# Optimization experiments

Measured on AMD Instinct MI355X. Metric: run time of the kernel, lower is better.

## Reference

```python
import jax, jax.numpy as jnp
import numpy as np

# Model hyperparameters (from init_kwargs)
D_MODEL, D_STATE, D_CONV, EXPAND, NHEADS, NGROUPS = 1024, 16, 4, 2, 8, 1
D_INNER = D_MODEL * EXPAND                      # 2048
HEADDIM = D_INNER // NHEADS                     # 256
D_XBC = D_INNER + 2 * NGROUPS * D_STATE         # conv channels: x + B + C
D_IN_PROJ = 3 * D_INNER + D_XBC + NHEADS        # z0 + x0 + z(unused) + xBC + dt
BATCH, SEQLEN = 2, 2048
LN_EPS = 1e-5


def setup_inputs() -> dict:
    key = jax.random.key(0)
    ks = jax.random.split(key, 8)
    u = jax.random.normal(ks[0], (BATCH, SEQLEN, D_MODEL), dtype=jnp.float32)
    W_in = jax.random.normal(ks[1], (D_IN_PROJ, D_MODEL), jnp.float32) / np.sqrt(D_MODEL)
    conv_w = jax.random.normal(ks[2], (D_XBC, 1, D_CONV), jnp.float32) / np.sqrt(D_CONV)
    conv_b = jnp.zeros((D_XBC,), jnp.float32)
    # dt_bias = inverse-softplus of dt ~ LogUniform(1e-3, 1e-1), as in source init
    dt = jnp.exp(jax.random.uniform(ks[3], (NHEADS,)) * (np.log(0.1) - np.log(0.001)) + np.log(0.001))
    dt_bias = dt + jnp.log(-jnp.expm1(-dt))
    A_log = jnp.log(jax.random.uniform(ks[4], (NHEADS,), minval=0.9, maxval=0.999))
    D_param = jnp.ones((NHEADS,), jnp.float32)
    ln_gamma = jnp.ones((D_INNER,), jnp.float32)
    ln_beta = jnp.zeros((D_INNER,), jnp.float32)
    W_gate = jax.random.normal(ks[5], (D_INNER, D_INNER), jnp.float32) / np.sqrt(D_INNER)
    b_gate = jnp.zeros((D_INNER,), jnp.float32)
    W_out = jax.random.normal(ks[6], (D_MODEL, 2 * D_INNER), jnp.float32) / np.sqrt(2 * D_INNER)
    return dict(u=u, W_in=W_in, conv_w=conv_w, conv_b=conv_b, dt_bias=dt_bias,
                A_log=A_log, D_param=D_param, ln_gamma=ln_gamma, ln_beta=ln_beta,
                W_gate=W_gate, b_gate=b_gate, W_out=W_out)


def _silu(x):
    return x * jax.nn.sigmoid(x)


def reference(u, W_in, conv_w, conv_b, dt_bias, A_log, D_param,
              ln_gamma, ln_beta, W_gate, b_gate, W_out):
    B, L, _ = u.shape
    zxbcdt = u @ W_in.T                                   # [B,L,D_IN_PROJ]
    z0 = zxbcdt[..., :D_INNER]
    x0 = zxbcdt[..., D_INNER:2 * D_INNER]
    # z = zxbcdt[..., 2*D_INNER:3*D_INNER]  # split but never used in source forward
    xBC = zxbcdt[..., 3 * D_INNER:3 * D_INNER + D_XBC]
    dt = jax.nn.softplus(zxbcdt[..., -NHEADS:] + dt_bias)  # [B,L,H]
    A = -jnp.exp(A_log)                                    # [H], per-head scalar

    # causal depthwise conv1d over time (left pad d_conv-1, crop to L)
    xBC_c = jnp.transpose(xBC, (0, 2, 1))                  # [B,C,L]
    xBC_c = jax.lax.conv_general_dilated(
        xBC_c, conv_w, window_strides=(1,), padding=[(D_CONV - 1, 0)],
        dimension_numbers=('NCH', 'OIH', 'NCH'), feature_group_count=D_XBC)
    xBC = _silu(jnp.transpose(xBC_c, (0, 2, 1)) + conv_b)  # [B,L,C]

    x = xBC[..., :D_INNER].reshape(B, L, NHEADS, HEADDIM)  # [B,L,H,P]
    Bm = xBC[..., D_INNER:D_INNER + D_STATE]               # [B,L,N] (ngroups=1)
    Cm = xBC[..., D_INNER + D_STATE:]                      # [B,L,N]

    def step(h, inp):
        x_t, B_t, C_t, dt_t = inp                          # [B,H,P],[B,N],[B,N],[B,H]
        dA = jnp.exp(dt_t * A)[:, :, None, None]           # [B,H,1,1]
        h = dA * h + (dt_t[:, :, None, None] * x_t[..., None]) * B_t[:, None, None, :]
        y_t = jnp.einsum('bhpn,bn->bhp', h, C_t) + D_param[None, :, None] * x_t
        return h, y_t

    h0 = jnp.zeros((B, NHEADS, HEADDIM, D_STATE), u.dtype)
    xs = (jnp.moveaxis(x, 1, 0), jnp.moveaxis(Bm, 1, 0),
          jnp.moveaxis(Cm, 1, 0), jnp.moveaxis(dt, 1, 0))
    _, y = jax.lax.scan(step, h0, xs)                      # [L,B,H,P]
    y = jnp.moveaxis(y, 0, 1).reshape(B, L, D_INNER)

    # LayerNorm
    mu = y.mean(-1, keepdims=True)
    var = ((y - mu) ** 2).mean(-1, keepdims=True)
    y = (y - mu) * jax.lax.rsqrt(var + LN_EPS) * ln_gamma + ln_beta

    gate = jax.nn.sigmoid(y @ W_gate.T + b_gate)
    y = gate * y

    mlp_skip = _silu(z0) * x0
    return jnp.concatenate([mlp_skip, y], axis=-1) @ W_out.T  # [B,L,D_MODEL]
```

## Files before the change

### kernel.cpp

```cpp
#include <hip/hip_runtime.h>
#include <hip/hip_bf16.h>
#include <math.h>

#define BATCH   2
#define SEQLEN  2048
#define DMODEL  1024
#define DINNER  2048
#define DSTATE  16
#define NHEADS  8
#define HEADDIM 256
#define DXBC    2080
#define NPACK   6184
#define NPAD    6400
#define MROWS   4096
#define CHUNK   64
#define NCHUNK  32
#define BH      16

typedef unsigned int u32;
typedef unsigned short u16;
typedef __attribute__((ext_vector_type(8))) short short8;
typedef __attribute__((ext_vector_type(4))) float f32x4;

#define GLOAD16(g, l) __builtin_amdgcn_global_load_lds( \
    (const __attribute__((address_space(1))) u32*)(g),  \
    (__attribute__((address_space(3))) u32*)(l), 16, 0, 0)

__device__ __forceinline__ u16 f2bf(float f) {
  union { float f; u32 u; } v; v.f = f;
  u32 r = v.u + 0x7fff + ((v.u >> 16) & 1);
  return (u16)(r >> 16);
}
__device__ __forceinline__ float bf2f(u16 b) {
  union { u32 u; float f; } v; v.u = ((u32)b) << 16;
  return v.f;
}

struct GParts { float* p0; float* p1; };

#define S_U   1048576
#define S_WG  1048576
#define S_WO  1048576
#define S_WP  1638400
#define S_TOT (S_U + S_WG + S_WO + S_WP)

__global__ void cvt_all(const float* __restrict__ u, const float* __restrict__ Wg,
                        const float* __restrict__ Wo, const float* __restrict__ Win,
                        u16* __restrict__ ub, u16* __restrict__ Wgb,
                        u16* __restrict__ Wob, u16* __restrict__ Wp) {
  for (int i = blockIdx.x * 256 + threadIdx.x; i < S_TOT; i += gridDim.x * 256) {
    const float* src; u16* dst; int idx;
    if (i < S_U) { src = u; dst = ub; idx = i; }
    else if (i < S_U + S_WG) { src = Wg; dst = Wgb; idx = i - S_U; }
    else if (i < S_U + S_WG + S_WO) { src = Wo; dst = Wob; idx = i - S_U - S_WG; }
    else {
      int j = i - S_U - S_WG - S_WO;
      int row = j >> 8, c4 = j & 255;
      ushort4 o = make_ushort4(0, 0, 0, 0);
      if (row < NPACK) {
        int orig = row < 4096 ? row : row + 2048;
        float4 v = ((const float4*)(Win + (size_t)orig * DMODEL))[c4];
        o = make_ushort4(f2bf(v.x), f2bf(v.y), f2bf(v.z), f2bf(v.w));
      }
      ((ushort4*)Wp)[j] = o;
      continue;
    }
    float4 v = ((const float4*)src)[idx];
    ((ushort4*)dst)[idx] = make_ushort4(f2bf(v.x), f2bf(v.y), f2bf(v.z), f2bf(v.w));
  }
}


template <int BMT>
__device__ __forceinline__ void stage32(const u16* __restrict__ Ag,
                                        const u16* __restrict__ Bg,
                                        int ldk, char* buf, int w, int l) {
  const int rr = w * 16 + (l >> 2);
  const int kc = (l & 3) * 8;
  #pragma unroll
  for (int j = 0; j < BMT / 128; ++j)
    GLOAD16(Ag + (size_t)(j * 128 + rr) * ldk + kc, buf + j * 8192 + w * 1024);
  #pragma unroll
  for (int j = 0; j < 2; ++j)
    GLOAD16(Bg + (size_t)(j * 128 + rr) * ldk + kc, buf + BMT * 64 + j * 8192 + w * 1024);
}

template <int EPI, int BMT>
__global__ __launch_bounds__(512, 1) void gemm256(
    const u16* __restrict__ A, const u16* __restrict__ B, int K_loop, int ldk, int ldo,
    void* __restrict__ outp, const float* __restrict__ bias,
    const u16* __restrict__ gate_in, GParts gp) {
  constexpr int ABYTES = BMT * 64;
  constexpr int TBYTES = ABYTES + 16384;
  constexpr int MREP   = BMT / 32;
  __shared__ char lds[4 * TBYTES];
  const int tid = threadIdx.x;
  const int w = tid >> 6, l = tid & 63;
  const int wm = w >> 2, wn = w & 3;
  const int fr = l & 15, g = l >> 4;
  int s = blockIdx.y * gridDim.x + blockIdx.x;
  const int nwg = gridDim.x * gridDim.y;
  s = (s & 7) * (nwg >> 3) + (s >> 3);
  const int bx = s % gridDim.x, by = s / gridDim.x;
  const u16* Ap = A + (size_t)bx * BMT * ldk + (size_t)blockIdx.z * K_loop;
  const u16* Bp = B + (size_t)by * 256 * ldk + (size_t)blockIdx.z * K_loop;
  const int NT = K_loop >> 5;

  f32x4 acc[MREP][4];
  #pragma unroll
  for (int m = 0; m < MREP; ++m)
    #pragma unroll
    for (int n = 0; n < 4; ++n) acc[m][n] = (f32x4){0.f, 0.f, 0.f, 0.f};

  stage32<BMT>(Ap,      Bp,      ldk, lds,              w, l);
  stage32<BMT>(Ap + 32, Bp + 32, ldk, lds + TBYTES,     w, l);
  stage32<BMT>(Ap + 64, Bp + 64, ldk, lds + 2 * TBYTES, w, l);
  if constexpr (BMT == 256) asm volatile("s_waitcnt vmcnt(8)" ::: "memory");
  else                      asm volatile("s_waitcnt vmcnt(6)" ::: "memory");
  __builtin_amdgcn_s_barrier();
  __builtin_amdgcn_sched_barrier(0);

  auto compute = [&](int t) {
    const char* cb = lds + (t & 3) * TBYTES;
    short8 bf[4];
    #pragma unroll
    for (int n = 0; n < 4; ++n)
      bf[n] = *(const short8*)(cb + ABYTES + (wn * 64 + n * 16 + fr) * 64 + g * 16);
    #pragma unroll
    for (int m = 0; m < MREP; ++m) {
      short8 am = *(const short8*)(cb + (wm * (BMT / 2) + m * 16 + fr) * 64 + g * 16);
      #pragma unroll
      for (int n = 0; n < 4; ++n)
        acc[m][n] = __builtin_amdgcn_mfma_f32_16x16x32_bf16(am, bf[n], acc[m][n], 0, 0, 0);
    }
  };

  int t = 0;
  for (; t < NT - 3; ++t) {
    stage32<BMT>(Ap + (size_t)(t + 3) * 32, Bp + (size_t)(t + 3) * 32, ldk,
                 lds + ((t + 3) & 3) * TBYTES, w, l);
    __builtin_amdgcn_sched_barrier(0);
    compute(t);
    if constexpr (BMT == 256) asm volatile("s_waitcnt vmcnt(8)" ::: "memory");
    else                      asm volatile("s_waitcnt vmcnt(6)" ::: "memory");
    __builtin_amdgcn_s_barrier();
    __builtin_amdgcn_sched_barrier(0);
  }
  compute(t);
  if constexpr (BMT == 256) asm volatile("s_waitcnt vmcnt(4)" ::: "memory");
  else                      asm volatile("s_waitcnt vmcnt(3)" ::: "memory");
  __builtin_amdgcn_s_barrier();
  __builtin_amdgcn_sched_barrier(0);
  compute(t + 1);
  asm volatile("s_waitcnt vmcnt(0)" ::: "memory");
  __builtin_amdgcn_s_barrier();
  __builtin_amdgcn_sched_barrier(0);
  compute(t + 2);

  const int er = (l >> 4) * 4, ec = l & 15;
  float* pp = nullptr;
  if (EPI == 2) pp = blockIdx.z == 0 ? gp.p0 : gp.p1;
  #pragma unroll
  for (int m = 0; m < MREP; ++m) {
    #pragma unroll
    for (int n = 0; n < 4; ++n) {
      #pragma unroll
      for (int j = 0; j < 4; ++j) {
        int row = bx * BMT + wm * (BMT / 2) + m * 16 + er + j;
        int col = by * 256 + wn * 64 + n * 16 + ec;
        float v = acc[m][n][j];
        if (EPI == 0) {
          ((u16*)outp)[(size_t)row * ldo + col] = f2bf(v);
        } else if (EPI == 1) {
          float gt = 1.f / (1.f + __expf(-(v + bias[col])));
          float nv = bf2f(gate_in[(size_t)row * 2048 + col]);
          ((u16*)outp)[(size_t)row * 4096 + 2048 + col] = f2bf(gt * nv);
        } else {
          pp[(size_t)row * ldo + col] = v;
        }
      }
    }
  }
}

__global__ void reduce2(const float* __restrict__ p0, const float* __restrict__ p1,
                        float* __restrict__ out) {
  const int n4 = MROWS * DMODEL / 4;
  for (int i = blockIdx.x * 256 + threadIdx.x; i < n4; i += gridDim.x * 256) {
    float4 a = ((const float4*)p0)[i];
    float4 b = ((const float4*)p1)[i];
    float4 o;
    o.x = a.x + b.x; o.y = a.y + b.y; o.z = a.z + b.z; o.w = a.w + b.w;
    ((float4*)out)[i] = o;
  }
}

#define NB_CONV 33280
#define NB_MLP  8192
#define NB_DT   128

__global__ void prep_kernel(const u16* __restrict__ zx, const float* __restrict__ cw,
                            const float* __restrict__ cb, u16* __restrict__ xc,
                            float* __restrict__ bc, u16* __restrict__ hcat,
                            const float* __restrict__ dt_bias, float* __restrict__ dtb) {
  int blk = blockIdx.x;
  if (blk < NB_CONV) {
    int idx = blk * 256 + threadIdx.x;
    if (idx >= MROWS * DXBC) return;
    int c = idx % DXBC;
    int m = idx / DXBC;
    int l = m & (SEQLEN - 1);
    float acc = cb[c];
    float w0 = cw[c * 4 + 0], w1 = cw[c * 4 + 1], w2 = cw[c * 4 + 2], w3 = cw[c * 4 + 3];
    const u16* col = zx + (size_t)m * NPAD + 4096 + c;
    acc += w3 * bf2f(col[0]);
    if (l >= 1) acc += w2 * bf2f(col[-NPAD]);
    if (l >= 2) acc += w1 * bf2f(col[-2 * NPAD]);
    if (l >= 3) acc += w0 * bf2f(col[-3 * NPAD]);
    float sv = acc / (1.f + __expf(-acc));
    if (c < DINNER) xc[(size_t)m * DINNER + c] = f2bf(sv);
    else bc[(size_t)m * 32 + (c - DINNER)] = sv;
  } else if (blk < NB_CONV + NB_MLP) {
    int i = (blk - NB_CONV) * 256 + threadIdx.x;
    int m = i >> 9, c4 = (i & 511) * 4;
    const u16* row = zx + (size_t)m * NPAD;
    ushort4 zv = *(const ushort4*)(row + c4);
    ushort4 xv = *(const ushort4*)(row + 2048 + c4);
    float z0, x0;
    ushort4 o;
    z0 = bf2f(zv.x); x0 = bf2f(xv.x); o.x = f2bf(x0 * z0 / (1.f + __expf(-z0)));
    z0 = bf2f(zv.y); x0 = bf2f(xv.y); o.y = f2bf(x0 * z0 / (1.f + __expf(-z0)));
    z0 = bf2f(zv.z); x0 = bf2f(xv.z); o.z = f2bf(x0 * z0 / (1.f + __expf(-z0)));
    z0 = bf2f(zv.w); x0 = bf2f(xv.w); o.w = f2bf(x0 * z0 / (1.f + __expf(-z0)));
    *(ushort4*)(hcat + (size_t)m * 4096 + c4) = o;
  } else {
    int idx = (blk - NB_CONV - NB_MLP) * 256 + threadIdx.x;
    if (idx >= MROWS * NHEADS) return;
    int hd = idx & 7, m = idx >> 3;
    float raw = bf2f(zx[(size_t)m * NPAD + 6176 + hd]) + dt_bias[hd];
    float dtv = raw > 20.f ? raw : log1pf(expf(raw));
    dtb[idx] = dtv;
  }
}

__device__ __forceinline__ int xs_addr(int r, int p) {
  return r * 512 + ((((p >> 3) ^ ((r >> 3) & 3)) & 31) << 4) + (p & 7) * 2;
}
__device__ __forceinline__ int P_addr(int t, int s) {
  return t * 128 + ((((s >> 3) ^ (t & 7)) & 7) << 4) + (s & 7) * 2;
}

__device__ __forceinline__ void stage_x(u16* xs, const u16* __restrict__ xc,
                                        size_t base, int tid) {
  #pragma unroll
  for (int it = 0; it < 8; ++it) {
    int r = it * 8 + (tid >> 5);
    int pc = (tid & 31) * 8;
    short8 v = *(const short8*)(xc + base + (size_t)r * DINNER + pc);
    *(short8*)((char*)xs + xs_addr(r, pc)) = v;
  }
}

__device__ __forceinline__ short8 xfrag(const u16* xs, int k0, int g, int p) {
  short8 v;
  #pragma unroll
  for (int j = 0; j < 8; ++j) {
    int s = k0 + g * 8 + j;
    v[j] = *(const short*)((const char*)xs + xs_addr(s, p));
  }
  return v;
}

__global__ __launch_bounds__(256) void ssd_state(
    const u16* __restrict__ xc, const float* __restrict__ bcb,
    const float* __restrict__ dtb, const float* __restrict__ A_log,
    float* __restrict__ Sbuf, float* __restrict__ lcbuf) {
  __shared__ u16 xs[64 * 256];
  __shared__ float sLC[64], sDT[64];
  __shared__ float wBT[16][65];
  const int tid = threadIdx.x;
  const int bh = blockIdx.x >> 5, c = blockIdx.x & 31;
  const int b = bh >> 3, h = bh & 7;
  const size_t row0 = (size_t)b * SEQLEN + c * CHUNK;
  stage_x(xs, xc, row0 * DINNER + h * HEADDIM, tid);
  if (tid < 64) {
    float dtv = dtb[(row0 + tid) * NHEADS + h];
    float A = -__expf(A_log[h]);
    float s = dtv * A;
    #pragma unroll
    for (int off = 1; off < 64; off <<= 1) {
      float v = __shfl_up(s, off, 64);
      if (tid >= off) s += v;
    }
    sLC[tid] = s; sDT[tid] = dtv;
    lcbuf[(size_t)blockIdx.x * 64 + tid] = s;
  }
  __syncthreads();
  const float lc63 = sLC[63];
  for (int i = tid; i < 1024; i += 256) {
    int n = i & 15, t = i >> 4;
    float w = sDT[t] * __expf(lc63 - sLC[t]);
    wBT[n][t] = w * bcb[(row0 + t) * 32 + n];
  }
  __syncthreads();
  const int lane = tid & 63, w = tid >> 6;
  const int cl = lane & 15, g = lane >> 4;
  f32x4 acc[4];
  #pragma unroll
  for (int pt = 0; pt < 4; ++pt) acc[pt] = (f32x4){0.f, 0.f, 0.f, 0.f};
  #pragma unroll
  for (int kk = 0; kk < 2; ++kk) {
    int k0 = kk * 32;
    short8 af;
    #pragma unroll
    for (int j = 0; j < 8; ++j) af[j] = (short)f2bf(wBT[cl][k0 + g * 8 + j]);
    #pragma unroll
    for (int pt = 0; pt < 4; ++pt) {
      short8 bf = xfrag(xs, k0, g, (w * 4 + pt) * 16 + cl);
      acc[pt] = __builtin_amdgcn_mfma_f32_16x16x32_bf16(af, bf, acc[pt], 0, 0, 0);
    }
  }
  float* Sc = Sbuf + (size_t)blockIdx.x * 16 * 256;
  #pragma unroll
  for (int pt = 0; pt < 4; ++pt)
    #pragma unroll
    for (int j = 0; j < 4; ++j)
      Sc[(g * 4 + j) * 256 + (w * 4 + pt) * 16 + cl] = acc[pt][j];
}

__global__ __launch_bounds__(256) void ssd_combine(
    const float* __restrict__ Sbuf, const float* __restrict__ lcbuf,
    float* __restrict__ Sprev) {
  const int bh = blockIdx.x >> 4, seg = blockIdx.x & 15;
  const int idx = seg * 256 + threadIdx.x;
  float r = 0.f;
  #pragma unroll 1
  for (int c = 0; c < NCHUNK; ++c) {
    size_t o = ((size_t)bh * NCHUNK + c) * 4096 + idx;
    Sprev[o] = r;
    float lam = __expf(lcbuf[((size_t)bh * NCHUNK + c) * 64 + 63]);
    r = lam * r + Sbuf[o];
  }
}

__global__ __launch_bounds__(256) void ssd_out(
    const u16* __restrict__ xc, const float* __restrict__ bcb,
    const float* __restrict__ dtb, const float* __restrict__ lcbuf,
    const float* __restrict__ Sprev, const float* __restrict__ D_par,
    u16* __restrict__ y) {
  __shared__ u16 xs[64 * 256];
  __shared__ u16 P[64 * 64];
  __shared__ u16 sB[64][17], sC[64][17], sCe[64][17];
  __shared__ u16 sSp[256][17];
  __shared__ float sLC[64], sDT[64];
  const int tid = threadIdx.x;
  const int bh = blockIdx.x >> 5, c = blockIdx.x & 31;
  const int b = bh >> 3, h = bh & 7;
  const size_t row0 = (size_t)b * SEQLEN + c * CHUNK;
  stage_x(xs, xc, row0 * DINNER + h * HEADDIM, tid);
  if (tid < 64) {
    sLC[tid] = lcbuf[(size_t)blockIdx.x * 64 + tid];
    sDT[tid] = dtb[(row0 + tid) * NHEADS + h];
  }
  for (int i = tid; i < 1024; i += 256) {
    int n = i & 15, t = i >> 4;
    float Bv = bcb[(row0 + t) * 32 + n];
    float Cv = bcb[(row0 + t) * 32 + 16 + n];
    float e = __expf(lcbuf[(size_t)blockIdx.x * 64 + t]);
    sB[t][n] = f2bf(Bv);
    sC[t][n] = f2bf(Cv);
    sCe[t][n] = f2bf(Cv * e);
  }
  {
    const float* Sp = Sprev + (size_t)blockIdx.x * 4096;
    int p = tid & 255;
    if (tid < 256) {
      #pragma unroll
      for (int n = 0; n < 16; ++n) sSp[p][n] = f2bf(Sp[n * 256 + p]);
    }
  }
  __syncthreads();

  const int lane = tid & 63, w = tid >> 6;
  const int cl = lane & 15, g = lane >> 4;

  f32x4 gacc[4];
  #pragma unroll
  for (int st = 0; st < 4; ++st) gacc[st] = (f32x4){0.f, 0.f, 0.f, 0.f};
  short8 afc = (short8){0, 0, 0, 0, 0, 0, 0, 0};
  if (g < 2) {
    #pragma unroll
    for (int j = 0; j < 8; ++j) afc[j] = (short)sC[w * 16 + cl][g * 8 + j];
  }
  #pragma unroll
  for (int st = 0; st < 4; ++st) {
    short8 bfb = (short8){0, 0, 0, 0, 0, 0, 0, 0};
    if (g < 2) {
      #pragma unroll
      for (int j = 0; j < 8; ++j) bfb[j] = (short)sB[st * 16 + cl][g * 8 + j];
    }
    gacc[st] = __builtin_amdgcn_mfma_f32_16x16x32_bf16(afc, bfb, gacc[st], 0, 0, 0);
  }
  #pragma unroll
  for (int st = 0; st < 4; ++st) {
    #pragma unroll
    for (int j = 0; j < 4; ++j) {
      int t = w * 16 + g * 4 + j;
      int s = st * 16 + cl;
      float v = 0.f;
      if (s <= t) v = gacc[st][j] * sDT[s] * __expf(sLC[t] - sLC[s]);
      *(u16*)((char*)P + P_addr(t, s)) = f2bf(v);
    }
  }
  asm volatile("s_waitcnt lgkmcnt(0)" ::: "memory");
  __builtin_amdgcn_sched_barrier(0);

  f32x4 acc[16];
  #pragma unroll
  for (int pt = 0; pt < 16; ++pt) acc[pt] = (f32x4){0.f, 0.f, 0.f, 0.f};
  #pragma unroll
  for (int kk = 0; kk < 2; ++kk) {
    int k0 = kk * 32;
    short8 ap = *(const short8*)((const char*)P + P_addr(w * 16 + cl, k0 + g * 8));
    #pragma unroll
    for (int pt = 0; pt < 16; ++pt) {
      short8 bf = xfrag(xs, k0, g, pt * 16 + cl);
      acc[pt] = __builtin_amdgcn_mfma_f32_16x16x32_bf16(ap, bf, acc[pt], 0, 0, 0);
    }
  }
  {
    short8 ae = (short8){0, 0, 0, 0, 0, 0, 0, 0};
    if (g < 2) {
      #pragma unroll
      for (int j = 0; j < 8; ++j) ae[j] = (short)sCe[w * 16 + cl][g * 8 + j];
    }
    #pragma unroll
    for (int pt = 0; pt < 16; ++pt) {
      short8 bs = (short8){0, 0, 0, 0, 0, 0, 0, 0};
      if (g < 2) {
        #pragma unroll
        for (int j = 0; j < 8; ++j) bs[j] = (short)sSp[pt * 16 + cl][g * 8 + j];
      }
      acc[pt] = __builtin_amdgcn_mfma_f32_16x16x32_bf16(ae, bs, acc[pt], 0, 0, 0);
    }
  }
  const float Dv = D_par[h];
  #pragma unroll
  for (int pt = 0; pt < 16; ++pt) {
    #pragma unroll
    for (int j = 0; j < 4; ++j) {
      int t = w * 16 + g * 4 + j;
      int p = pt * 16 + cl;
      float xv = bf2f(*(const u16*)((const char*)xs + xs_addr(t, p)));
      float v = acc[pt][j] + Dv * xv;
      y[(row0 + t) * DINNER + h * HEADDIM + p] = f2bf(v);
    }
  }
}

__global__ __launch_bounds__(256) void ln_kernel(const u16* __restrict__ y,
                                                 const float* __restrict__ gamma,
                                                 const float* __restrict__ beta,
                                                 u16* __restrict__ nrm) {
  const int row = blockIdx.x;
  const int t = threadIdx.x;
  const u16* yr = y + (size_t)row * DINNER;
  short8 v = *(const short8*)(yr + t * 8);
  float f[8];
  float s = 0.f, ss = 0.f;
  #pragma unroll
  for (int j = 0; j < 8; ++j) {
    f[j] = bf2f((u16)v[j]);
    s += f[j]; ss += f[j] * f[j];
  }
  #pragma unroll
  for (int o = 1; o < 64; o <<= 1) { s += __shfl_xor(s, o); ss += __shfl_xor(ss, o); }
  __shared__ float rs[4], rss[4];
  const int wid = t >> 6;
  if ((t & 63) == 0) { rs[wid] = s; rss[wid] = ss; }
  __syncthreads();
  s = rs[0] + rs[1] + rs[2] + rs[3];
  ss = rss[0] + rss[1] + rss[2] + rss[3];
  float mu = s * (1.f / DINNER);
  float var = ss * (1.f / DINNER) - mu * mu;
  float inv = rsqrtf(var + 1e-5f);
  float4 g0 = ((const float4*)gamma)[t * 2], g1 = ((const float4*)gamma)[t * 2 + 1];
  float4 b0 = ((const float4*)beta)[t * 2], b1 = ((const float4*)beta)[t * 2 + 1];
  short8 o;
  o[0] = (short)f2bf((f[0] - mu) * inv * g0.x + b0.x);
  o[1] = (short)f2bf((f[1] - mu) * inv * g0.y + b0.y);
  o[2] = (short)f2bf((f[2] - mu) * inv * g0.z + b0.z);
  o[3] = (short)f2bf((f[3] - mu) * inv * g0.w + b0.w);
  o[4] = (short)f2bf((f[4] - mu) * inv * g1.x + b1.x);
  o[5] = (short)f2bf((f[5] - mu) * inv * g1.y + b1.y);
  o[6] = (short)f2bf((f[6] - mu) * inv * g1.z + b1.z);
  o[7] = (short)f2bf((f[7] - mu) * inv * g1.w + b1.w);
  *(short8*)(nrm + (size_t)row * DINNER + t * 8) = o;
}

extern "C" void kernel_launch(void* const* d_in, const int* in_sizes, int n_in,
                              void* d_out, int out_size, void* d_ws, size_t ws_size,
                              hipStream_t stream) {
  (void)in_sizes; (void)n_in; (void)out_size; (void)ws_size;
  const float* u       = (const float*)d_in[0];
  const float* W_in    = (const float*)d_in[1];
  const float* conv_w  = (const float*)d_in[2];
  const float* conv_b  = (const float*)d_in[3];
  const float* dt_bias = (const float*)d_in[4];
  const float* A_log   = (const float*)d_in[5];
  const float* D_par   = (const float*)d_in[6];
  const float* ln_g    = (const float*)d_in[7];
  const float* ln_b    = (const float*)d_in[8];
  const float* W_gate  = (const float*)d_in[9];
  const float* b_gate  = (const float*)d_in[10];
  const float* W_out   = (const float*)d_in[11];
  float* out = (float*)d_out;

  size_t off = 0;
  auto take = [&](size_t bytes) -> char* {
    char* p = (char*)d_ws + off;
    off = (off + bytes + 255) & ~(size_t)255;
    return p;
  };
  u16* u16b  = (u16*)take((size_t)MROWS * DMODEL * 2);
  u16* Wp    = (u16*)take((size_t)NPAD * DMODEL * 2);
  u16* Wg    = (u16*)take((size_t)DINNER * DINNER * 2);
  u16* Wo    = (u16*)take((size_t)DMODEL * 2 * DINNER * 2);
  u16* zx    = (u16*)take((size_t)MROWS * NPAD * 2);
  u16* xc    = (u16*)take((size_t)MROWS * DINNER * 2);
  float* bcb = (float*)take((size_t)MROWS * 32 * 4);
  float* dtb = (float*)take((size_t)MROWS * NHEADS * 4);
  float* lcbuf = (float*)take((size_t)BH * NCHUNK * 64 * 4);
  u16* nrm   = (u16*)take((size_t)MROWS * DINNER * 2);
  u16* hcat  = (u16*)take((size_t)MROWS * 2 * DINNER * 2);

  float* Sbuf  = (float*)u16b;
  u16*   y     = zx;
  float* Sprev = (float*)((char*)zx + (size_t)16 * 1024 * 1024);
  GParts parts2;
  parts2.p0 = (float*)zx;
  parts2.p1 = (float*)((char*)zx + (size_t)16 * 1024 * 1024);
  GParts none = {nullptr, nullptr};

  cvt_all<<<4096, 256, 0, stream>>>(u, W_gate, W_out, W_in, u16b, Wg, Wo, Wp);

  gemm256<0, 256><<<dim3(MROWS / 256, NPAD / 256, 1), 512, 0, stream>>>(
      u16b, Wp, DMODEL, DMODEL, NPAD, zx, nullptr, nullptr, none);

  prep_kernel<<<NB_CONV + NB_MLP + NB_DT, 256, 0, stream>>>(
      zx, conv_w, conv_b, xc, bcb, hcat, dt_bias, dtb);

  ssd_state<<<BH * NCHUNK, 256, 0, stream>>>(xc, bcb, dtb, A_log, Sbuf, lcbuf);
  ssd_combine<<<BH * 16, 256, 0, stream>>>(Sbuf, lcbuf, Sprev);
  ssd_out<<<BH * NCHUNK, 256, 0, stream>>>(xc, bcb, dtb, lcbuf, Sprev, D_par, y);

  ln_kernel<<<MROWS, 256, 0, stream>>>(y, ln_g, ln_b, nrm);

  gemm256<1, 128><<<dim3(MROWS / 128, DINNER / 256, 1), 512, 0, stream>>>(
      nrm, Wg, DINNER, DINNER, 0, hcat, b_gate, nrm, none);

  gemm256<2, 128><<<dim3(MROWS / 128, DMODEL / 256, 2), 512, 0, stream>>>(
      hcat, Wo, 2 * DINNER / 2, 2 * DINNER, DMODEL, nullptr, nullptr, nullptr, parts2);

  reduce2<<<2048, 256, 0, stream>>>(parts2.p0, parts2.p1, out);
}
```

Baseline: 256.9 us.

## Rewrite GEMM kernels with K=64 swizzled LDS tiles and interleaved staging

Replaces the generic 4-stage K=32 GEMM with two specialised kernels. The in-projection GEMM uses a double-buffered K=64 tile and an XOR-swizzled LDS layout. It interleaves global-to-LDS loads for the next tile between MFMA groups and raises wave priority during MFMA bursts. The gate and out-proj GEMMs switch to 256x128 tiles with a 3-stage K=64 pipeline. The aim is fewer barriers, fewer LDS bank conflicts and better load/compute overlap, at the cost of more complex vmcnt bookkeeping and a different wave tiling.

```diff
diff --git a/kernel.cpp b/kernel.cpp
--- a/kernel.cpp
+++ b/kernel.cpp
@@ -25,6 +25,8 @@
 #define GLOAD16(g, l) __builtin_amdgcn_global_load_lds( \
     (const __attribute__((address_space(1))) u32*)(g),  \
     (__attribute__((address_space(3))) u32*)(l), 16, 0, 0)
+
+#define MFMA_B16(d, a, b) d = __builtin_amdgcn_mfma_f32_16x16x32_bf16(a, b, d, 0, 0, 0)
 
 __device__ __forceinline__ u16 f2bf(float f) {
   union { float f; u32 u; } v; v.f = f;
@@ -70,30 +72,26 @@
   }
 }
 
-
-template <int BMT>
-__device__ __forceinline__ void stage32(const u16* __restrict__ Ag,
-                                        const u16* __restrict__ Bg,
-                                        int ldk, char* buf, int w, int l) {
-  const int rr = w * 16 + (l >> 2);
-  const int kc = (l & 3) * 8;
-  #pragma unroll
-  for (int j = 0; j < BMT / 128; ++j)
-    GLOAD16(Ag + (size_t)(j * 128 + rr) * ldk + kc, buf + j * 8192 + w * 1024);
-  #pragma unroll
-  for (int j = 0; j < 2; ++j)
-    GLOAD16(Bg + (size_t)(j * 128 + rr) * ldk + kc, buf + BMT * 64 + j * 8192 + w * 1024);
-}
-
-template <int EPI, int BMT>
-__global__ __launch_bounds__(512, 1) void gemm256(
-    const u16* __restrict__ A, const u16* __restrict__ B, int K_loop, int ldk, int ldo,
-    void* __restrict__ outp, const float* __restrict__ bias,
-    const u16* __restrict__ gate_in, GParts gp) {
-  constexpr int ABYTES = BMT * 64;
-  constexpr int TBYTES = ABYTES + 16384;
-  constexpr int MREP   = BMT / 32;
-  __shared__ char lds[4 * TBYTES];
+template <int NL>
+__device__ __forceinline__ void stage_rows(const u16* __restrict__ gsrc, int ldk,
+                                           char* ldsmat, int row0, int w, int l) {
+  const int rl = w * 8 + (l >> 3);
+  const int q = ((l & 7) ^ (l >> 3)) * 8;
+  #pragma unroll
+  for (int j = 0; j < NL; ++j) {
+    GLOAD16(gsrc + (size_t)(row0 + j * 64 + rl) * ldk + q,
+            ldsmat + (row0 + j * 64 + w * 8) * 128);
+  }
+}
+
+__device__ __forceinline__ short8 frag8(const char* mat, int row, int q) {
+  return *(const short8*)(mat + row * 128 + ((q ^ (row & 7)) << 4));
+}
+
+__global__ __launch_bounds__(512, 1) void gemmA(
+    const u16* __restrict__ A, const u16* __restrict__ B, int K, int ldk,
+    int ldo, u16* __restrict__ outp) {
+  __shared__ char lds[131072];
   const int tid = threadIdx.x;
   const int w = tid >> 6, l = tid & 63;
   const int wm = w >> 2, wn = w & 3;
@@ -102,76 +100,236 @@
   const int nwg = gridDim.x * gridDim.y;
   s = (s & 7) * (nwg >> 3) + (s >> 3);
   const int bx = s % gridDim.x, by = s / gridDim.x;
-  const u16* Ap = A + (size_t)bx * BMT * ldk + (size_t)blockIdx.z * K_loop;
-  const u16* Bp = B + (size_t)by * 256 * ldk + (size_t)blockIdx.z * K_loop;
-  const int NT = K_loop >> 5;
-
-  f32x4 acc[MREP][4];
-  #pragma unroll
-  for (int m = 0; m < MREP; ++m)
+  const u16* Ap = A + (size_t)bx * 256 * ldk;
+  const u16* Bp = B + (size_t)by * 256 * ldk;
+  const int NT = K >> 6;
+
+  f32x4 acc[8][4];
+  #pragma unroll
+  for (int m = 0; m < 8; ++m)
     #pragma unroll
     for (int n = 0; n < 4; ++n) acc[m][n] = (f32x4){0.f, 0.f, 0.f, 0.f};
 
-  stage32<BMT>(Ap,      Bp,      ldk, lds,              w, l);
-  stage32<BMT>(Ap + 32, Bp + 32, ldk, lds + TBYTES,     w, l);
-  stage32<BMT>(Ap + 64, Bp + 64, ldk, lds + 2 * TBYTES, w, l);
-  if constexpr (BMT == 256) asm volatile("s_waitcnt vmcnt(8)" ::: "memory");
-  else                      asm volatile("s_waitcnt vmcnt(6)" ::: "memory");
-  __builtin_amdgcn_s_barrier();
-  __builtin_amdgcn_sched_barrier(0);
-
-  auto compute = [&](int t) {
-    const char* cb = lds + (t & 3) * TBYTES;
-    short8 bf[4];
-    #pragma unroll
-    for (int n = 0; n < 4; ++n)
-      bf[n] = *(const short8*)(cb + ABYTES + (wn * 64 + n * 16 + fr) * 64 + g * 16);
-    #pragma unroll
-    for (int m = 0; m < MREP; ++m) {
-      short8 am = *(const short8*)(cb + (wm * (BMT / 2) + m * 16 + fr) * 64 + g * 16);
-      #pragma unroll
-      for (int n = 0; n < 4; ++n)
-        acc[m][n] = __builtin_amdgcn_mfma_f32_16x16x32_bf16(am, bf[n], acc[m][n], 0, 0, 0);
-    }
-  };
-
-  int t = 0;
-  for (; t < NT - 3; ++t) {
-    stage32<BMT>(Ap + (size_t)(t + 3) * 32, Bp + (size_t)(t + 3) * 32, ldk,
-                 lds + ((t + 3) & 3) * TBYTES, w, l);
-    __builtin_amdgcn_sched_barrier(0);
-    compute(t);
-    if constexpr (BMT == 256) asm volatile("s_waitcnt vmcnt(8)" ::: "memory");
-    else                      asm volatile("s_waitcnt vmcnt(6)" ::: "memory");
+  stage_rows<2>(Bp, ldk, lds + 32768, 0, w, l);
+  stage_rows<2>(Bp, ldk, lds + 32768, 128, w, l);
+  stage_rows<1>(Ap, ldk, lds, 0, w, l);
+  stage_rows<1>(Ap, ldk, lds, 128, w, l);
+  stage_rows<1>(Ap, ldk, lds, 64, w, l);
+  stage_rows<1>(Ap, ldk, lds, 192, w, l);
+
+  for (int t = 0; t < NT; ++t) {
+    const bool last = (t == NT - 1);
+    const char* cbA = lds + (t & 1) * 65536;
+    const char* cbB = cbA + 32768;
+    char* nbA = lds + ((t + 1) & 1) * 65536;
+    char* nbB = nbA + 32768;
+    const u16* An = Ap + (size_t)(t + 1) * 64;
+    const u16* Bn = Bp + (size_t)(t + 1) * 64;
+
+    asm volatile("s_waitcnt vmcnt(2)" ::: "memory");
     __builtin_amdgcn_s_barrier();
     __builtin_amdgcn_sched_barrier(0);
-  }
-  compute(t);
-  if constexpr (BMT == 256) asm volatile("s_waitcnt vmcnt(4)" ::: "memory");
-  else                      asm volatile("s_waitcnt vmcnt(3)" ::: "memory");
-  __builtin_amdgcn_s_barrier();
-  __builtin_amdgcn_sched_barrier(0);
-  compute(t + 1);
-  asm volatile("s_waitcnt vmcnt(0)" ::: "memory");
-  __builtin_amdgcn_s_barrier();
-  __builtin_amdgcn_sched_barrier(0);
-  compute(t + 2);
-
-  const int er = (l >> 4) * 4, ec = l & 15;
+
+    short8 bf0[4], bf1[4];
+    #pragma unroll
+    for (int n = 0; n < 4; ++n) {
+      bf0[n] = frag8(cbB, wn * 64 + n * 16 + fr, g);
+      bf1[n] = frag8(cbB, wn * 64 + n * 16 + fr, 4 + g);
+    }
+    {
+      short8 a00 = frag8(cbA, wm * 128 + fr, g);
+      short8 a01 = frag8(cbA, wm * 128 + fr, 4 + g);
+      short8 a10 = frag8(cbA, wm * 128 + 16 + fr, g);
+      short8 a11 = frag8(cbA, wm * 128 + 16 + fr, 4 + g);
+      if (!last) stage_rows<2>(Bn, ldk, nbB, 0, w, l);
+      asm volatile("s_waitcnt lgkmcnt(0)" ::: "memory");
+      __builtin_amdgcn_sched_barrier(0);
+      __builtin_amdgcn_s_setprio(1);
+      #pragma unroll
+      for (int n = 0; n < 4; ++n) { MFMA_B16(acc[0][n], a00, bf0[n]); MFMA_B16(acc[1][n], a10, bf0[n]); }
+      #pragma unroll
+      for (int n = 0; n < 4; ++n) { MFMA_B16(acc[0][n], a01, bf1[n]); MFMA_B16(acc[1][n], a11, bf1[n]); }
+      __builtin_amdgcn_s_setprio(0);
+    }
+    {
+      short8 a00 = frag8(cbA, wm * 128 + 32 + fr, g);
+      short8 a01 = frag8(cbA, wm * 128 + 32 + fr, 4 + g);
+      short8 a10 = frag8(cbA, wm * 128 + 48 + fr, g);
+      short8 a11 = frag8(cbA, wm * 128 + 48 + fr, 4 + g);
+      if (!last) stage_rows<2>(Bn, ldk, nbB, 128, w, l);
+      asm volatile("s_waitcnt lgkmcnt(0)" ::: "memory");
+      __builtin_amdgcn_sched_barrier(0);
+      __builtin_amdgcn_s_setprio(1);
+      #pragma unroll
+      for (int n = 0; n < 4; ++n) { MFMA_B16(acc[2][n], a00, bf0[n]); MFMA_B16(acc[3][n], a10, bf0[n]); }
+      #pragma unroll
+      for (int n = 0; n < 4; ++n) { MFMA_B16(acc[2][n], a01, bf1[n]); MFMA_B16(acc[3][n], a11, bf1[n]); }
+      __builtin_amdgcn_s_setprio(0);
+    }
+    if (last) { asm volatile("s_waitcnt vmcnt(0)" ::: "memory"); }
+    else      { asm volatile("s_waitcnt vmcnt(4)" ::: "memory"); }
+    __builtin_amdgcn_s_barrier();
+    __builtin_amdgcn_sched_barrier(0);
+    {
+      short8 a00 = frag8(cbA, wm * 128 + 64 + fr, g);
+      short8 a01 = frag8(cbA, wm * 128 + 64 + fr, 4 + g);
+      short8 a10 = frag8(cbA, wm * 128 + 80 + fr, g);
+      short8 a11 = frag8(cbA, wm * 128 + 80 + fr, 4 + g);
+      if (!last) { stage_rows<1>(An, ldk, nbA, 0, w, l); stage_rows<1>(An, ldk, nbA, 128, w, l); }
+      asm volatile("s_waitcnt lgkmcnt(0)" ::: "memory");
+      __builtin_amdgcn_sched_barrier(0);
+      __builtin_amdgcn_s_setprio(1);
+      #pragma unroll
+      for (int n = 0; n < 4; ++n) { MFMA_B16(acc[4][n], a00, bf0[n]); MFMA_B16(acc[5][n], a10, bf0[n]); }
+      #pragma unroll
+      for (int n = 0; n < 4; ++n) { MFMA_B16(acc[4][n], a01, bf1[n]); MFMA_B16(acc[5][n], a11, bf1[n]); }
+      __builtin_amdgcn_s_setprio(0);
+    }
+    {
+      short8 a00 = frag8(cbA, wm * 128 + 96 + fr, g);
+      short8 a01 = frag8(cbA, wm * 128 + 96 + fr, 4 + g);
+      short8 a10 = frag8(cbA, wm * 128 + 112 + fr, g);
+      short8 a11 = frag8(cbA, wm * 128 + 112 + fr, 4 + g);
+      if (!last) { stage_rows<1>(An, ldk, nbA, 64, w, l); stage_rows<1>(An, ldk, nbA, 192, w, l); }
+      asm volatile("s_waitcnt lgkmcnt(0)" ::: "memory");
+      __builtin_amdgcn_sched_barrier(0);
+      __builtin_amdgcn_s_setprio(1);
+      #pragma unroll
+      for (int n = 0; n < 4; ++n) { MFMA_B16(acc[6][n], a00, bf0[n]); MFMA_B16(acc[7][n], a10, bf0[n]); }
+      #pragma unroll
+      for (int n = 0; n < 4; ++n) { MFMA_B16(acc[6][n], a01, bf1[n]); MFMA_B16(acc[7][n], a11, bf1[n]); }
+      __builtin_amdgcn_s_setprio(0);
+    }
+  }
+
+  const int er = g * 4;
+  #pragma unroll
+  for (int m = 0; m < 8; ++m)
+    #pragma unroll
+    for (int n = 0; n < 4; ++n)
+      #pragma unroll
+      for (int j = 0; j < 4; ++j) {
+        int row = bx * 256 + wm * 128 + m * 16 + er + j;
+        int col = by * 256 + wn * 64 + n * 16 + fr;
+        outp[(size_t)row * ldo + col] = f2bf(acc[m][n][j]);
+      }
+}
+
+template <int EPI>
+__global__ __launch_bounds__(512, 1) void gemmB(
+    const u16* __restrict__ A, const u16* __restrict__ B, int K_loop, int ldk,
+    int ldo, void* __restrict__ outp, const float* __restrict__ bias,
+    const u16* __restrict__ gate_in, GParts gp) {
+  __shared__ char lds[3 * 49152];
+  const int tid = threadIdx.x;
+  const int w = tid >> 6, l = tid & 63;
+  const int wm = w >> 1, wn = w & 1;
+  const int fr = l & 15, g = l >> 4;
+  int s = blockIdx.y * gridDim.x + blockIdx.x;
+  const int nwg = gridDim.x * gridDim.y;
+  s = (s & 7) * (nwg >> 3) + (s >> 3);
+  const int bx = s % gridDim.x, by = s / gridDim.x;
+  const u16* Ap = A + (size_t)bx * 256 * ldk + (size_t)blockIdx.z * K_loop;
+  const u16* Bp = B + (size_t)by * 128 * ldk + (size_t)blockIdx.z * K_loop;
+  const int NT = K_loop >> 6;
+
+  f32x4 acc[4][4];
+  #pragma unroll
+  for (int m = 0; m < 4; ++m)
+    #pragma unroll
+    for (int n = 0; n < 4; ++n) acc[m][n] = (f32x4){0.f, 0.f, 0.f, 0.f};
+
+  #pragma unroll
+  for (int p = 0; p < 2; ++p) {
+    char* bA = lds + p * 49152;
+    char* bB = bA + 32768;
+    const u16* Ak = Ap + (size_t)p * 64;
+    const u16* Bk = Bp + (size_t)p * 64;
+    stage_rows<1>(Bk, ldk, bB, 0, w, l);
+    stage_rows<1>(Bk, ldk, bB, 64, w, l);
+    stage_rows<1>(Ak, ldk, bA, 0, w, l);
+    stage_rows<1>(Ak, ldk, bA, 64, w, l);
+    stage_rows<1>(Ak, ldk, bA, 128, w, l);
+    stage_rows<1>(Ak, ldk, bA, 192, w, l);
+  }
+
+  int cur = 0;
+  for (int t = 0; t < NT; ++t) {
+    const bool last = (t == NT - 1);
+    const bool dostage = (t + 2 < NT);
+    int st = cur + 2; if (st >= 3) st -= 3;
+    const char* cbA = lds + cur * 49152;
+    const char* cbB = cbA + 32768;
+    char* nbA = lds + st * 49152;
+    char* nbB = nbA + 32768;
+    const u16* An = Ap + (size_t)(t + 2) * 64;
+    const u16* Bn = Bp + (size_t)(t + 2) * 64;
+
+    if (last) { asm volatile("s_waitcnt vmcnt(0)" ::: "memory"); }
+    else      { asm volatile("s_waitcnt vmcnt(6)" ::: "memory"); }
+    __builtin_amdgcn_s_barrier();
+    __builtin_amdgcn_sched_barrier(0);
+
+    short8 bf0[4], bf1[4];
+    #pragma unroll
+    for (int n = 0; n < 4; ++n) {
+      bf0[n] = frag8(cbB, wn * 64 + n * 16 + fr, g);
+      bf1[n] = frag8(cbB, wn * 64 + n * 16 + fr, 4 + g);
+    }
+    {
+      short8 a00 = frag8(cbA, wm * 64 + fr, g);
+      short8 a01 = frag8(cbA, wm * 64 + fr, 4 + g);
+      short8 a10 = frag8(cbA, wm * 64 + 16 + fr, g);
+      short8 a11 = frag8(cbA, wm * 64 + 16 + fr, 4 + g);
+      if (dostage) {
+        stage_rows<1>(Bn, ldk, nbB, 0, w, l);
+        stage_rows<1>(Bn, ldk, nbB, 64, w, l);
+        stage_rows<1>(An, ldk, nbA, 0, w, l);
+      }
+      asm volatile("s_waitcnt lgkmcnt(0)" ::: "memory");
+      __builtin_amdgcn_sched_barrier(0);
+      __builtin_amdgcn_s_setprio(1);
+      #pragma unroll
+      for (int n = 0; n < 4; ++n) { MFMA_B16(acc[0][n], a00, bf0[n]); MFMA_B16(acc[1][n], a10, bf0[n]); }
+      #pragma unroll
+      for (int n = 0; n < 4; ++n) { MFMA_B16(acc[0][n], a01, bf1[n]); MFMA_B16(acc[1][n], a11, bf1[n]); }
+      __builtin_amdgcn_s_setprio(0);
+    }
+    {
+      short8 a00 = frag8(cbA, wm * 64 + 32 + fr, g);
+      short8 a01 = frag8(cbA, wm * 64 + 32 + fr, 4 + g);
+      short8 a10 = frag8(cbA, wm * 64 + 48 + fr, g);
+      short8 a11 = frag8(cbA, wm * 64 + 48 + fr, 4 + g);
+      if (dostage) {
+        stage_rows<1>(An, ldk, nbA, 64, w, l);
+        stage_rows<1>(An, ldk, nbA, 128, w, l);
+        stage_rows<1>(An, ldk, nbA, 192, w, l);
+      }
+      asm volatile("s_waitcnt lgkmcnt(0)" ::: "memory");
+      __builtin_amdgcn_sched_barrier(0);
+      __builtin_amdgcn_s_setprio(1);
+      #pragma unroll
+      for (int n = 0; n < 4; ++n) { MFMA_B16(acc[2][n], a00, bf0[n]); MFMA_B16(acc[3][n], a10, bf0[n]); }
+      #pragma unroll
+      for (int n = 0; n < 4; ++n) { MFMA_B16(acc[2][n], a01, bf1[n]); MFMA_B16(acc[3][n], a11, bf1[n]); }
+      __builtin_amdgcn_s_setprio(0);
+    }
+    cur = cur + 1; if (cur >= 3) cur = 0;
+  }
+
+  const int er = g * 4;
   float* pp = nullptr;
   if (EPI == 2) pp = blockIdx.z == 0 ? gp.p0 : gp.p1;
   #pragma unroll
-  for (int m = 0; m < MREP; ++m) {
-    #pragma unroll
-    for (int n = 0; n < 4; ++n) {
+  for (int m = 0; m < 4; ++m)
+    #pragma unroll
+    for (int n = 0; n < 4; ++n)
       #pragma unroll
       for (int j = 0; j < 4; ++j) {
-        int row = bx * BMT + wm * (BMT / 2) + m * 16 + er + j;
-        int col = by * 256 + wn * 64 + n * 16 + ec;
+        int row = bx * 256 + wm * 64 + m * 16 + er + j;
+        int col = by * 128 + wn * 64 + n * 16 + fr;
         float v = acc[m][n][j];
-        if (EPI == 0) {
-          ((u16*)outp)[(size_t)row * ldo + col] = f2bf(v);
-        } else if (EPI == 1) {
+        if (EPI == 1) {
           float gt = 1.f / (1.f + __expf(-(v + bias[col])));
           float nv = bf2f(gate_in[(size_t)row * 2048 + col]);
           ((u16*)outp)[(size_t)row * 4096 + 2048 + col] = f2bf(gt * nv);
@@ -179,8 +337,6 @@
           pp[(size_t)row * ldo + col] = v;
         }
       }
-    }
-  }
 }
 
 __global__ void reduce2(const float* __restrict__ p0, const float* __restrict__ p1,
@@ -544,8 +700,8 @@
 
   cvt_all<<<4096, 256, 0, stream>>>(u, W_gate, W_out, W_in, u16b, Wg, Wo, Wp);
 
-  gemm256<0, 256><<<dim3(MROWS / 256, NPAD / 256, 1), 512, 0, stream>>>(
-      u16b, Wp, DMODEL, DMODEL, NPAD, zx, nullptr, nullptr, none);
+  gemmA<<<dim3(MROWS / 256, NPAD / 256), 512, 0, stream>>>(
+      u16b, Wp, DMODEL, DMODEL, NPAD, zx);
 
   prep_kernel<<<NB_CONV + NB_MLP + NB_DT, 256, 0, stream>>>(
       zx, conv_w, conv_b, xc, bcb, hcat, dt_bias, dtb);
@@ -556,10 +712,10 @@
 
   ln_kernel<<<MROWS, 256, 0, stream>>>(y, ln_g, ln_b, nrm);
 
-  gemm256<1, 128><<<dim3(MROWS / 128, DINNER / 256, 1), 512, 0, stream>>>(
+  gemmB<1><<<dim3(MROWS / 256, DINNER / 128), 512, 0, stream>>>(
       nrm, Wg, DINNER, DINNER, 0, hcat, b_gate, nrm, none);
 
-  gemm256<2, 128><<<dim3(MROWS / 128, DMODEL / 256, 2), 512, 0, stream>>>(
+  gemmB<2><<<dim3(MROWS / 256, DMODEL / 128, 2), 512, 0, stream>>>(
       hcat, Wo, 2 * DINNER / 2, 2 * DINNER, DMODEL, nullptr, nullptr, nullptr, parts2);
 
   reduce2<<<2048, 256, 0, stream>>>(parts2.p0, parts2.p1, out);
```

Measured after the change: 252.7 us. Within noise of the previous version (-1.6%).
